# Optimization experiments

Measured on AMD Instinct MI355X. Metric: run time of the kernel, lower is better.

## Reference

```python
import jax, jax.numpy as jnp
from jax import lax
import numpy as np

B, V, H, K, E = 256, 30000, 512, 200, 300
SH_ALPHA = 20.0
REC_W = 0.7
N_ITERS = 100       # fixed iteration budget (original caps at 5000; convergence check freezes updates)
STOP_THR = 0.005
BN_EPS = 1e-3


def setup_inputs() -> dict:
    key = jax.random.key(0)
    ks = jax.random.split(key, 8)
    n = lambda k, shape, scale: (jax.random.normal(k, shape, jnp.float32) * scale)
    return {
        "bows": jax.random.uniform(ks[0], (B, V), jnp.float32),
        "W1": n(ks[1], (H, V), 0.01),
        "b1": jnp.zeros((H,), jnp.float32),
        "W2": n(ks[2], (K, H), 0.05),
        "b2": jnp.zeros((K,), jnp.float32),
        "gamma": jnp.ones((K,), jnp.float32),
        "beta": jnp.zeros((K,), jnp.float32),
        "word_emb": n(ks[3], (V, E), 0.1),
        "topic_emb": n(ks[4], (K, E), 0.1),
    }


def _l2norm(x):
    return x / jnp.maximum(jnp.linalg.norm(x, axis=1, keepdims=True), 1e-12)


def _sinkhorn(cost, kernel, a, b):
    # a: [K,B], b: [V,B], kernel: [K,V]
    u0 = jnp.ones_like(a) / a.shape[0]
    v0 = jnp.ones_like(b)

    def body(carry, i):
        u, v, err = carry
        active = err > STOP_THR
        # u = a / (kernel @ (b / (u^T kernel)^T))
        u1 = a / (kernel @ (b / (u.T @ kernel).T))

        def check(_):
            v1 = b / (kernel.T @ u1)
            u2 = a / (kernel @ v1)
            bb = v1 * (kernel.T @ u2)
            e = jnp.max(jnp.sum(jnp.abs(bb - b), axis=0))
            return u2, v1, e

        # original does the v-refresh + err check when steps % 20 == 1 (steps = i+1)
        u1, v1, e1 = lax.cond(i % 20 == 0, check, lambda _: (u1, v, err), None)
        u = jnp.where(active, u1, u)
        v = jnp.where(active, v1, v)
        err = jnp.where(active, e1, err)
        return (u, v, err), None

    (u, v, _), _ = lax.scan(jax.checkpoint(body), (u0, v0, jnp.asarray(1.0, a.dtype)),
                            jnp.arange(N_ITERS))
    # per-document sinkhorn cost: sum_k u * ((kernel*cost) @ v)
    return jnp.sum(u * ((kernel * cost) @ v), axis=0)  # [B]


def reference(bows, W1, b1, W2, b2, gamma, beta, word_emb, topic_emb):
    # encoder (training-mode BN with batch stats; dropout disabled for determinism)
    h = jax.nn.relu(bows @ W1.T + b1)                      # [B,H]
    z = h @ W2.T + b2                                      # [B,K]
    mu = jnp.mean(z, axis=0)
    var = jnp.var(z, axis=0)                               # biased, as torch BN uses
    zn = gamma * (z - mu) / jnp.sqrt(var + BN_EPS) + beta
    doc_topic = jax.nn.softmax(zn, axis=1)                 # [B,K]

    topic_word = _l2norm(topic_emb) @ _l2norm(word_emb).T  # [K,V]
    cost = 1.0 - topic_word
    kernel = jnp.exp(-cost * SH_ALPHA)

    doc_word = jax.nn.softmax(bows, axis=1)                # [B,V]
    sinkhorn_loss = _sinkhorn(cost, kernel, doc_topic.T, doc_word.T).mean()

    rec_log_probs = jax.nn.log_softmax(doc_topic @ topic_word, axis=1)  # [B,V]
    reconstruction_loss = -(rec_log_probs * bows).sum(axis=1).mean()
    return REC_W * reconstruction_loss, sinkhorn_loss
```

## Files before the change

### kernel.cpp

```cpp
#include <hip/hip_runtime.h>
#include <math.h>

#define CDIV(a,b) (((a)+(b)-1)/(b))

typedef unsigned short u16;
typedef unsigned long long u64;
typedef __attribute__((ext_vector_type(8))) short bf16x8;
typedef __attribute__((ext_vector_type(4))) float f32x4;

constexpr int Bn = 256;
constexpr int Vn = 30000;
constexpr int Hn = 512;
constexpr int Kn = 200;
constexpr int En = 300;
constexpr int Kp = 224;
constexpr int Vc = 224;
constexpr int NCH = 135;
constexpr int Vpad = NCH * Vc;
constexpr float ALPHA  = 20.0f;
constexpr float RECW   = 0.7f;
constexpr float THRC   = 0.005f;
constexpr float EPS_BN = 1e-3f;
constexpr int   NIT    = 100;

__device__ __forceinline__ float bf2f(u16 h) {
  union { unsigned u; float f; } c; c.u = (unsigned)h << 16; return c.f;
}
__device__ __forceinline__ u16 f2bf(float f) {
  union { float f; unsigned u; } c; c.f = f;
  return (u16)((c.u + 0x7fffu + ((c.u >> 16) & 1u)) >> 16);
}

template<int MODE>
__global__ __launch_bounds__(256, 2)
void fusedAB(const u16* __restrict__ kernT, const u16* __restrict__ kernA,
             const u16* __restrict__ ub, const u16* __restrict__ bmb,
             u16* __restrict__ wout, const u16* __restrict__ win,
             u16* __restrict__ tpart, float* __restrict__ errp,
             const int* __restrict__ frozen)
{
  if (MODE != 3 && frozen[0]) return;
  const int c = blockIdx.x, g = blockIdx.y;
  const int v0 = c * Vc, b0 = g * 64;
  const int tid = threadIdx.x;
  const int wv = tid >> 6, l = tid & 63, l15 = l & 15, lg = l >> 4;
  const int rloc = wv * 16 + l15;
  const int bcol = b0 + rloc;
  __shared__ u16 wlds[64 * Vc];
  char* wbase = (char*)wlds;
  const int sw = (rloc & 3) << 4;

  if (MODE != 3) {
    bf16x8 uf[7];
    {
      const u16* up = ub + (size_t)bcol * Kp + lg * 8;
#pragma unroll
      for (int ks = 0; ks < 7; ++ks) uf[ks] = *(const bf16x8*)(up + ks * 32);
    }
    float e = 0.f;
    for (int vt = 0; vt < Vc / 16; ++vt) {
      const u16* ktp = kernT + (size_t)(v0 + vt * 16 + l15) * Kp + lg * 8;
      f32x4 acc = {0.f, 0.f, 0.f, 0.f};
#pragma unroll
      for (int ks = 0; ks < 7; ++ks) {
        bf16x8 kf = *(const bf16x8*)(ktp + ks * 32);
        acc = __builtin_amdgcn_mfma_f32_16x16x32_bf16(kf, uf[ks], acc, 0, 0, 0);
      }
      const int vbase = v0 + vt * 16 + lg * 4;
      const size_t po = (size_t)bcol * Vpad + vbase;
      u64 bq = *(const u64*)(bmb + po);
      if (MODE == 2) {
        u64 wq = *(const u64*)(win + po);
#pragma unroll
        for (int r = 0; r < 4; ++r) {
          float bm = bf2f((u16)(bq >> (16 * r)));
          float wv_ = bf2f((u16)(wq >> (16 * r)));
          e += fabsf(wv_ * acc[r] - bm);
        }
      } else {
        u64 wq = 0;
#pragma unroll
        for (int r = 0; r < 4; ++r) {
          float bm = bf2f((u16)(bq >> (16 * r)));
          float w = (vbase + r < Vn) ? bm / acc[r] : 0.f;
          wq |= (u64)f2bf(w) << (16 * r);
        }
        *(u64*)(wbase + rloc * (Vc * 2) + ((vt * 32 + lg * 8) ^ sw)) = wq;
        if (MODE == 1) *(u64*)(wout + po) = wq;
      }
    }
    if (MODE == 2) {
      e += __shfl_xor(e, 16, 64);
      e += __shfl_xor(e, 32, 64);
      if (l < 16) errp[c * Bn + bcol] = e;
      return;
    }
    __syncthreads();
  }

  f32x4 accB[13];
#pragma unroll
  for (int mt = 0; mt < 13; ++mt) accB[mt] = (f32x4){0.f, 0.f, 0.f, 0.f};
  for (int vs = 0; vs < Vc / 32; ++vs) {
    bf16x8 wf;
    if (MODE == 3) wf = *(const bf16x8*)(win + (size_t)bcol * Vpad + v0 + vs * 32 + lg * 8);
    else wf = *(const bf16x8*)(wbase + rloc * (Vc * 2) + (((vs * 32 + lg * 8) * 2) ^ sw));
    const u16* kap = kernA + (size_t)l15 * Vpad + v0 + vs * 32 + lg * 8;
#pragma unroll
    for (int mt = 0; mt < 13; ++mt) {
      bf16x8 af = *(const bf16x8*)(kap + (size_t)mt * 16 * Vpad);
      accB[mt] = __builtin_amdgcn_mfma_f32_16x16x32_bf16(af, wf, accB[mt], 0, 0, 0);
    }
  }
#pragma unroll
  for (int mt = 0; mt < 13; ++mt) {
#pragma unroll
    for (int r = 0; r < 4; ++r) {
      int k = mt * 16 + lg * 4 + r;
      if (k < Kn) tpart[((size_t)c * Kn + k) * Bn + bcol] = f2bf(accB[mt][r]);
    }
  }
}

__global__ __launch_bounds__(256, 2)
void reconMF(const u16* __restrict__ costT, const u16* __restrict__ dtb,
             u16* __restrict__ rbuf)
{
  const int c = blockIdx.x, g = blockIdx.y;
  const int v0 = c * Vc, b0 = g * 64;
  const int tid = threadIdx.x;
  const int wv = tid >> 6, l = tid & 63, l15 = l & 15, lg = l >> 4;
  const int bcol = b0 + wv * 16 + l15;
  bf16x8 uf[7];
  {
    const u16* up = dtb + (size_t)bcol * Kp + lg * 8;
#pragma unroll
    for (int ks = 0; ks < 7; ++ks) uf[ks] = *(const bf16x8*)(up + ks * 32);
  }
  for (int vt = 0; vt < Vc / 16; ++vt) {
    const u16* ktp = costT + (size_t)(v0 + vt * 16 + l15) * Kp + lg * 8;
    f32x4 acc = {0.f, 0.f, 0.f, 0.f};
#pragma unroll
    for (int ks = 0; ks < 7; ++ks) {
      bf16x8 kf = *(const bf16x8*)(ktp + ks * 32);
      acc = __builtin_amdgcn_mfma_f32_16x16x32_bf16(kf, uf[ks], acc, 0, 0, 0);
    }
    const int vbase = v0 + vt * 16 + lg * 4;
    u64 q = 0;
#pragma unroll
    for (int r = 0; r < 4; ++r) q |= (u64)f2bf(1.f - acc[r]) << (16 * r);
    *(u64*)(rbuf + (size_t)bcol * Vpad + vbase) = q;
  }
}

__global__ void prepKern(const float* __restrict__ P, u16* __restrict__ kern_bf,
                         u16* __restrict__ kc_bf, u16* __restrict__ cost_bf)
{
  int k = blockIdx.y;
  int v = blockIdx.x * 256 + threadIdx.x;
  if (v >= Vpad) return;
  float cf = 0.f, kf = 0.f;
  if (k < Kn && v < Vn) {
    cf = 1.f - P[(size_t)k * Vn + v];
    kf = expf(-ALPHA * cf);
  }
  size_t o = (size_t)k * Vpad + v;
  kern_bf[o] = f2bf(kf);
  kc_bf[o]   = f2bf(kf * cf);
  cost_bf[o] = f2bf(cf);
}

__global__ void transposeK(const u16* __restrict__ src, u16* __restrict__ dst)
{
  __shared__ u16 t[32][33];
  int tx = threadIdx.x & 31, ty = threadIdx.x >> 5;
  int v0 = blockIdx.x * 32, k0 = blockIdx.y * 32;
#pragma unroll
  for (int r = 0; r < 4; ++r) t[ty + 8 * r][tx] = src[(size_t)(k0 + ty + 8 * r) * Vpad + v0 + tx];
  __syncthreads();
#pragma unroll
  for (int r = 0; r < 4; ++r) dst[(size_t)(v0 + ty + 8 * r) * Kp + k0 + tx] = t[tx][ty + 8 * r];
}

__global__ __launch_bounds__(256)
void gemm_nt(const float* __restrict__ A, const float* __restrict__ Bm,
             const float* __restrict__ rsA, const float* __restrict__ rsB,
             float* __restrict__ P, int M, int N, int Kd)
{
  const int S = gridDim.z, s = blockIdx.z;
  const int k0 = (int)((long long)Kd * s / S);
  const int k1 = (int)((long long)Kd * (s + 1) / S);
  const int m0 = blockIdx.y * 64, n0 = blockIdx.x * 64;
  __shared__ float As[16][68];
  __shared__ float Bs[16][68];
  const int tid = threadIdx.x;
  const int tx = tid & 15, ty = tid >> 4;
  const int lrow = tid >> 2, lkg = (tid & 3) * 4;
  const int mi = m0 + lrow, ni = n0 + lrow;
  float acc[4][4] = {};
  for (int kc = k0; kc < k1; kc += 16) {
    float4 a4 = {0.f, 0.f, 0.f, 0.f}, b4 = {0.f, 0.f, 0.f, 0.f};
    if (kc + 16 <= k1) {
      if (mi < M) a4 = *(const float4*)&A[(size_t)mi * Kd + kc + lkg];
      if (ni < N) b4 = *(const float4*)&Bm[(size_t)ni * Kd + kc + lkg];
    } else {
      float ta[4] = {0.f, 0.f, 0.f, 0.f}, tb[4] = {0.f, 0.f, 0.f, 0.f};
      for (int jj = 0; jj < 4; ++jj) {
        int kk = kc + lkg + jj;
        if (kk < k1) {
          if (mi < M) ta[jj] = A[(size_t)mi * Kd + kk];
          if (ni < N) tb[jj] = Bm[(size_t)ni * Kd + kk];
        }
      }
      a4.x = ta[0]; a4.y = ta[1]; a4.z = ta[2]; a4.w = ta[3];
      b4.x = tb[0]; b4.y = tb[1]; b4.z = tb[2]; b4.w = tb[3];
    }
    if (rsA && mi < M) { float sc = rsA[mi]; a4.x *= sc; a4.y *= sc; a4.z *= sc; a4.w *= sc; }
    if (rsB && ni < N) { float sc = rsB[ni]; b4.x *= sc; b4.y *= sc; b4.z *= sc; b4.w *= sc; }
    As[lkg + 0][lrow] = a4.x; As[lkg + 1][lrow] = a4.y;
    As[lkg + 2][lrow] = a4.z; As[lkg + 3][lrow] = a4.w;
    Bs[lkg + 0][lrow] = b4.x; Bs[lkg + 1][lrow] = b4.y;
    Bs[lkg + 2][lrow] = b4.z; Bs[lkg + 3][lrow] = b4.w;
    __syncthreads();
#pragma unroll
    for (int kk = 0; kk < 16; ++kk) {
      float4 av = *(const float4*)&As[kk][ty * 4];
      float4 bv = *(const float4*)&Bs[kk][tx * 4];
      float a_[4] = {av.x, av.y, av.z, av.w};
      float b_[4] = {bv.x, bv.y, bv.z, bv.w};
#pragma unroll
      for (int i = 0; i < 4; ++i)
#pragma unroll
        for (int j = 0; j < 4; ++j)
          acc[i][j] += a_[i] * b_[j];
    }
    __syncthreads();
  }
  const size_t base = (size_t)s * M * N;
#pragma unroll
  for (int i = 0; i < 4; ++i) {
    int m = m0 + ty * 4 + i;
    if (m >= M) continue;
#pragma unroll
    for (int j = 0; j < 4; ++j) {
      int n = n0 + tx * 4 + j;
      if (n < N) P[base + (size_t)m * N + n] = acc[i][j];
    }
  }
}

__global__ void rowNorms(const float* __restrict__ X, float* __restrict__ rn, int R, int C)
{
  int wv = threadIdx.x >> 6, lane = threadIdx.x & 63;
  int r = blockIdx.x * 4 + wv;
  if (r >= R) return;
  float s = 0.f;
  for (int c = lane; c < C; c += 64) { float x = X[(size_t)r * C + c]; s += x * x; }
#pragma unroll
  for (int m = 32; m; m >>= 1) s += __shfl_xor(s, m, 64);
  if (lane == 0) rn[r] = 1.f / fmaxf(sqrtf(s), 1e-12f);
}

__global__ void epiH(const float* __restrict__ P, const float* __restrict__ b1,
                     float* __restrict__ h, int S)
{
  int i = blockIdx.x * blockDim.x + threadIdx.x;
  if (i >= Bn * Hn) return;
  float v = b1[i & (Hn - 1)];
  for (int s = 0; s < S; ++s) v += P[(size_t)s * Bn * Hn + i];
  h[i] = fmaxf(v, 0.f);
}

__global__ void bnStats(const float* __restrict__ P, const float* __restrict__ b2,
                        float* __restrict__ mu, float* __restrict__ ivar, int S)
{
  int k = blockIdx.x, b = threadIdx.x;
  float z = b2[k];
  for (int s = 0; s < S; ++s) z += P[((size_t)s * Bn + b) * Kn + k];
  __shared__ float r1[256], r2[256];
  r1[b] = z; r2[b] = z * z; __syncthreads();
  for (int st = 128; st; st >>= 1) {
    if (b < st) { r1[b] += r1[b + st]; r2[b] += r2[b + st]; }
    __syncthreads();
  }
  if (b == 0) {
    float m = r1[0] / Bn, v = r2[0] / Bn - (r1[0] / Bn) * (r1[0] / Bn);
    mu[k] = m; ivar[k] = rsqrtf(v + EPS_BN);
  }
}

__global__ void bnSoftmax(const float* __restrict__ P, const float* __restrict__ b2,
                          const float* __restrict__ mu, const float* __restrict__ ivar,
                          const float* __restrict__ gamma, const float* __restrict__ beta,
                          float* __restrict__ a, u16* __restrict__ dtb, int S)
{
  int b = blockIdx.x, k = threadIdx.x;
  float zn = -1e30f;
  if (k < Kn) {
    float z = b2[k];
    for (int s = 0; s < S; ++s) z += P[((size_t)s * Bn + b) * Kn + k];
    zn = gamma[k] * (z - mu[k]) * ivar[k] + beta[k];
  }
  __shared__ float red[256];
  red[k] = zn; __syncthreads();
  for (int st = 128; st; st >>= 1) { if (k < st) red[k] = fmaxf(red[k], red[k + st]); __syncthreads(); }
  float mx = red[0]; __syncthreads();
  float e = (k < Kn) ? expf(zn - mx) : 0.f;
  red[k] = e; __syncthreads();
  for (int st = 128; st; st >>= 1) { if (k < st) red[k] += red[k + st]; __syncthreads(); }
  float dt = e / red[0];
  if (k < Kn) a[(size_t)k * Bn + b] = dt;
  if (k < Kp) dtb[(size_t)b * Kp + k] = (k < Kn) ? f2bf(dt) : (u16)0;
}

__global__ __launch_bounds__(512)
void rowSoftmax2(const float* __restrict__ bows, u16* __restrict__ bmb)
{
  int b = blockIdx.x, t = threadIdx.x;
  const float4* row = (const float4*)(bows + (size_t)b * Vn);
  __shared__ float red[512];
  float mx = -1e30f;
  for (int v4 = t; v4 < Vn / 4; v4 += 512) {
    float4 x = row[v4];
    mx = fmaxf(mx, fmaxf(fmaxf(x.x, x.y), fmaxf(x.z, x.w)));
  }
  red[t] = mx; __syncthreads();
  for (int st = 256; st; st >>= 1) { if (t < st) red[t] = fmaxf(red[t], red[t + st]); __syncthreads(); }
  mx = red[0]; __syncthreads();
  float sum = 0.f;
  for (int v4 = t; v4 < Vn / 4; v4 += 512) {
    float4 x = row[v4];
    sum += expf(x.x - mx) + expf(x.y - mx) + expf(x.z - mx) + expf(x.w - mx);
  }
  red[t] = sum; __syncthreads();
  for (int st = 256; st; st >>= 1) { if (t < st) red[t] += red[t + st]; __syncthreads(); }
  float inv = 1.f / red[0];
  for (int v4 = t; v4 < Vn / 4; v4 += 512) {
    float4 x = row[v4];
    u64 q = (u64)f2bf(expf(x.x - mx) * inv)
          | ((u64)f2bf(expf(x.y - mx) * inv) << 16)
          | ((u64)f2bf(expf(x.z - mx) * inv) << 32)
          | ((u64)f2bf(expf(x.w - mx) * inv) << 48);
    *(u64*)(bmb + (size_t)b * Vpad + v4 * 4) = q;
  }
  for (int p = t; p < (Vpad - Vn) / 4; p += 512)
    *(u64*)(bmb + (size_t)b * Vpad + Vn + p * 4) = 0;
}

__global__ void initU2(float* __restrict__ u, u16* __restrict__ ub)
{
  int i = blockIdx.x * 256 + threadIdx.x;
  int k = i >> 8, b = i & 255;
  u[i] = 1.f / Kn;
  ub[(size_t)b * Kp + k] = f2bf(1.f / Kn);
  if (k < Kp - Kn) ub[(size_t)b * Kp + Kn + k] = 0;
}

__global__ void updateU2(const u16* __restrict__ tpart, const float* __restrict__ a,
                         float* __restrict__ u, u16* __restrict__ ub,
                         const int* __restrict__ frozen)
{
  if (frozen[0]) return;
  int i = blockIdx.x * 256 + threadIdx.x;
  float t = 0.f;
  for (int c = 0; c < NCH; ++c) t += bf2f(tpart[(size_t)c * Kn * Bn + i]);
  float uu = a[i] / t;
  u[i] = uu;
  int k = i >> 8, b = i & 255;
  ub[(size_t)b * Kp + k] = f2bf(uu);
  if (k < Kp - Kn) ub[(size_t)b * Kp + Kn + k] = 0;
}

__global__ void sumT(const u16* __restrict__ tpart, float* __restrict__ t2)
{
  int i = blockIdx.x * 256 + threadIdx.x;
  float t = 0.f;
  for (int c = 0; c < NCH; ++c) t += bf2f(tpart[(size_t)c * Kn * Bn + i]);
  t2[i] = t;
}

__global__ void errFin(const float* __restrict__ errp, int nc, int* __restrict__ frozen)
{
  if (frozen[0]) return;
  int b = threadIdx.x;
  float s = 0.f;
  for (int c = 0; c < nc; ++c) s += errp[(size_t)c * Bn + b];
  __shared__ float red[256];
  red[b] = s; __syncthreads();
  for (int st = 128; st; st >>= 1) { if (b < st) red[b] = fmaxf(red[b], red[b + st]); __syncthreads(); }
  if (b == 0 && red[0] <= THRC) frozen[0] = 1;
}

__global__ __launch_bounds__(512)
void recPass2(const u16* __restrict__ r, const float* __restrict__ bows,
              float* __restrict__ Lb)
{
  int b = blockIdx.x, t = threadIdx.x;
  const float m = 1.0f;
  const float4* br = (const float4*)(bows + (size_t)b * Vn);
  float se = 0.f, dot = 0.f, bs = 0.f;
  for (int v4 = t; v4 < Vn / 4; v4 += 512) {
    u64 q = *(const u64*)(r + (size_t)b * Vpad + v4 * 4);
    float4 w = br[v4];
    float x0 = bf2f((u16)q), x1 = bf2f((u16)(q >> 16));
    float x2 = bf2f((u16)(q >> 32)), x3 = bf2f((u16)(q >> 48));
    se  += expf(x0 - m) + expf(x1 - m) + expf(x2 - m) + expf(x3 - m);
    dot += w.x * x0 + w.y * x1 + w.z * x2 + w.w * x3;
    bs  += w.x + w.y + w.z + w.w;
  }
  __shared__ float red[512];
  red[t] = se; __syncthreads();
  for (int st = 256; st; st >>= 1) { if (t < st) red[t] += red[t + st]; __syncthreads(); }
  float seT = red[0]; __syncthreads();
  red[t] = dot; __syncthreads();
  for (int st = 256; st; st >>= 1) { if (t < st) red[t] += red[t + st]; __syncthreads(); }
  float dotT = red[0]; __syncthreads();
  red[t] = bs; __syncthreads();
  for (int st = 256; st; st >>= 1) { if (t < st) red[t] += red[t + st]; __syncthreads(); }
  if (t == 0) Lb[b] = dotT - (m + logf(seT)) * red[0];
}

__global__ void finalOut(const float* __restrict__ u, const float* __restrict__ t2,
                         const float* __restrict__ Lb, float* __restrict__ outp)
{
  int b = threadIdx.x;
  float sl = 0.f;
  for (int k = 0; k < Kn; ++k) sl += u[(size_t)k * Bn + b] * t2[(size_t)k * Bn + b];
  __shared__ float r1[256], r2[256];
  r1[b] = sl; r2[b] = Lb[b]; __syncthreads();
  for (int st = 128; st; st >>= 1) {
    if (b < st) { r1[b] += r1[b + st]; r2[b] += r2[b + st]; }
    __syncthreads();
  }
  if (b == 0) {
    outp[0] = RECW * (-(r2[0] / (float)Bn));
    outp[1] = r1[0] / (float)Bn;
  }
}

extern "C" void kernel_launch(void* const* d_in, const int* in_sizes, int n_in,
                              void* d_out, int out_size, void* d_ws, size_t ws_size,
                              hipStream_t stream)
{
  const float* bows  = (const float*)d_in[0];
  const float* W1    = (const float*)d_in[1];
  const float* b1    = (const float*)d_in[2];
  const float* W2    = (const float*)d_in[3];
  const float* b2    = (const float*)d_in[4];
  const float* gamma = (const float*)d_in[5];
  const float* beta  = (const float*)d_in[6];
  const float* wemb  = (const float*)d_in[7];
  const float* temb  = (const float*)d_in[8];
  float* out = (float*)d_out;

  float* ws = (float*)d_ws;
  size_t off = 0;
  auto alloc = [&](size_t n) { float* p = ws + off; off += (n + 63) & ~(size_t)63; return p; };
  float* wbuf    = alloc((size_t)Kn * Vn);
  u16*   kern_bf = (u16*)alloc(((size_t)Kp * Vpad + 1) / 2);
  u16*   kc_bf   = (u16*)alloc(((size_t)Kp * Vpad + 1) / 2);
  u16*   cost_bf = (u16*)alloc(((size_t)Kp * Vpad + 1) / 2);
  u16*   kernT   = (u16*)alloc(((size_t)Vpad * Kp + 1) / 2);
  u16*   costT   = (u16*)alloc(((size_t)Vpad * Kp + 1) / 2);
  u16*   bm_bf   = (u16*)alloc(((size_t)Bn * Vpad + 1) / 2);
  u16*   vb_bf   = (u16*)alloc(((size_t)Bn * Vpad + 1) / 2);
  u16*   rbuf    = (u16*)alloc(((size_t)Bn * Vpad + 1) / 2);
  u16*   ub_bf   = (u16*)alloc(((size_t)Bn * Kp + 1) / 2);
  u16*   dt_bf   = (u16*)alloc(((size_t)Bn * Kp + 1) / 2);
  u16*   tpart   = (u16*)alloc(((size_t)NCH * Kn * Bn + 1) / 2);
  float* hbuf    = alloc((size_t)Bn * Hn);
  float* abuf    = alloc((size_t)Kn * Bn);
  float* ubuf    = alloc((size_t)Kn * Bn);
  float* t2      = alloc((size_t)Kn * Bn);
  float* rnT     = alloc(Kn);
  float* rnW     = alloc(Vn);
  float* mu      = alloc(Kn);
  float* ivar    = alloc(Kn);
  float* errp    = alloc((size_t)NCH * Bn);
  float* Lb      = alloc(Bn);
  int* frozen = (int*)(ws + off); off += 64;
  if (off * sizeof(float) > ws_size) return;

  hipMemsetAsync(frozen, 0, sizeof(int), stream);

  rowNorms<<<CDIV(Kn, 4), 256, 0, stream>>>(temb, rnT, Kn, En);
  rowNorms<<<CDIV(Vn, 4), 256, 0, stream>>>(wemb, rnW, Vn, En);
  {
    dim3 g(CDIV(Vn, 64), CDIV(Kn, 64), 1);
    gemm_nt<<<g, 256, 0, stream>>>(temb, wemb, rnT, rnW, wbuf, Kn, Vn, En);
  }
  prepKern<<<dim3(CDIV(Vpad, 256), Kp), 256, 0, stream>>>(wbuf, kern_bf, kc_bf, cost_bf);
  transposeK<<<dim3(Vpad / 32, Kp / 32), 256, 0, stream>>>(kern_bf, kernT);
  transposeK<<<dim3(Vpad / 32, Kp / 32), 256, 0, stream>>>(cost_bf, costT);

  {
    dim3 g(CDIV(Hn, 64), CDIV(Bn, 64), 25);
    gemm_nt<<<g, 256, 0, stream>>>(bows, W1, nullptr, nullptr, wbuf, Bn, Hn, Vn);
  }
  epiH<<<CDIV(Bn * Hn, 256), 256, 0, stream>>>(wbuf, b1, hbuf, 25);
  {
    dim3 g(CDIV(Kn, 64), CDIV(Bn, 64), 4);
    gemm_nt<<<g, 256, 0, stream>>>(hbuf, W2, nullptr, nullptr, wbuf, Bn, Kn, Hn);
  }
  bnStats<<<Kn, 256, 0, stream>>>(wbuf, b2, mu, ivar, 4);
  bnSoftmax<<<Bn, 256, 0, stream>>>(wbuf, b2, mu, ivar, gamma, beta, abuf, dt_bf, 4);
  rowSoftmax2<<<Bn, 512, 0, stream>>>(bows, bm_bf);
  initU2<<<Kn, 256, 0, stream>>>(ubuf, ub_bf);

  dim3 gF(NCH, Bn / 64);
  for (int it = 0; it < NIT; ++it) {
    fusedAB<0><<<gF, 256, 0, stream>>>(kernT, kern_bf, ub_bf, bm_bf, nullptr, nullptr, tpart, nullptr, frozen);
    updateU2<<<Kn, 256, 0, stream>>>(tpart, abuf, ubuf, ub_bf, frozen);
    if (it % 20 == 0) {
      fusedAB<1><<<gF, 256, 0, stream>>>(kernT, kern_bf, ub_bf, bm_bf, vb_bf, nullptr, tpart, nullptr, frozen);
      updateU2<<<Kn, 256, 0, stream>>>(tpart, abuf, ubuf, ub_bf, frozen);
      fusedAB<2><<<gF, 256, 0, stream>>>(kernT, kern_bf, ub_bf, bm_bf, nullptr, vb_bf, tpart, errp, frozen);
      errFin<<<1, 256, 0, stream>>>(errp, NCH, frozen);
    }
  }

  reconMF<<<gF, 256, 0, stream>>>(costT, dt_bf, rbuf);
  recPass2<<<Bn, 512, 0, stream>>>(rbuf, bows, Lb);

  fusedAB<3><<<gF, 256, 0, stream>>>(kernT, kc_bf, ub_bf, bm_bf, nullptr, vb_bf, tpart, nullptr, frozen);
  sumT<<<Kn, 256, 0, stream>>>(tpart, t2);
  finalOut<<<1, 256, 0, stream>>>(ubuf, t2, Lb, out);
}
```

Measured before the change: 2.256 ms.

## Move setup GEMMs to bf16 MFMA, remap grids per XCD, vectorize u updates

The topic-word similarity GEMM now runs on MFMA using split hi/lo bf16 operands (three products) and fuses the kernel/cost epilogue, replacing the fp32 SIMT GEMM plus prepKern. The bows@W1 encoder GEMM moves to a bf16 MFMA split-K kernel. The sinkhorn fusedAB grid becomes 1D with chunk mapping grouped by XCD, NCH is padded to 136, and occupancy is raised to 3 blocks per CU. updateU2 and sumT read tpart with 64-bit vector loads, and the fp32 u copy is dropped in favour of the bf16 one. Workspace buffers are aliased to save memory. The trade-offs are bf16 rounding of the encoder inputs and a finalOut that now reads bf16 u.

```diff
diff --git a/kernel.cpp b/kernel.cpp
--- a/kernel.cpp
+++ b/kernel.cpp
@@ -13,10 +13,13 @@
 constexpr int Hn = 512;
 constexpr int Kn = 200;
 constexpr int En = 300;
+constexpr int E3 = 320;
 constexpr int Kp = 224;
 constexpr int Vc = 224;
-constexpr int NCH = 135;
+constexpr int NCH = 136;
+constexpr int CPX = NCH / 8;
 constexpr int Vpad = NCH * Vc;
+constexpr int SW1 = 32;
 constexpr float ALPHA  = 20.0f;
 constexpr float RECW   = 0.7f;
 constexpr float THRC   = 0.005f;
@@ -30,9 +33,18 @@
   union { float f; unsigned u; } c; c.f = f;
   return (u16)((c.u + 0x7fffu + ((c.u >> 16) & 1u)) >> 16);
 }
+__device__ __forceinline__ bf16x8 load8bf(const float* p) {
+  float4 a = *(const float4*)p, b = *(const float4*)(p + 4);
+  bf16x8 r;
+  r[0] = (short)f2bf(a.x); r[1] = (short)f2bf(a.y);
+  r[2] = (short)f2bf(a.z); r[3] = (short)f2bf(a.w);
+  r[4] = (short)f2bf(b.x); r[5] = (short)f2bf(b.y);
+  r[6] = (short)f2bf(b.z); r[7] = (short)f2bf(b.w);
+  return r;
+}
 
 template<int MODE>
-__global__ __launch_bounds__(256, 2)
+__global__ __launch_bounds__(256, 3)
 void fusedAB(const u16* __restrict__ kernT, const u16* __restrict__ kernA,
              const u16* __restrict__ ub, const u16* __restrict__ bmb,
              u16* __restrict__ wout, const u16* __restrict__ win,
@@ -40,7 +52,9 @@
              const int* __restrict__ frozen)
 {
   if (MODE != 3 && frozen[0]) return;
-  const int c = blockIdx.x, g = blockIdx.y;
+  const int bid = blockIdx.x;
+  const int xcd = bid & 7, wid = bid >> 3;
+  const int c = xcd * CPX + (wid >> 2), g = wid & 3;
   const int v0 = c * Vc, b0 = g * 64;
   const int tid = threadIdx.x;
   const int wv = tid >> 6, l = tid & 63, l15 = l & 15, lg = l >> 4;
@@ -153,21 +167,98 @@
   }
 }
 
-__global__ void prepKern(const float* __restrict__ P, u16* __restrict__ kern_bf,
-                         u16* __restrict__ kc_bf, u16* __restrict__ cost_bf)
-{
-  int k = blockIdx.y;
-  int v = blockIdx.x * 256 + threadIdx.x;
-  if (v >= Vpad) return;
-  float cf = 0.f, kf = 0.f;
-  if (k < Kn && v < Vn) {
-    cf = 1.f - P[(size_t)k * Vn + v];
-    kf = expf(-ALPHA * cf);
-  }
-  size_t o = (size_t)k * Vpad + v;
-  kern_bf[o] = f2bf(kf);
-  kc_bf[o]   = f2bf(kf * cf);
-  cost_bf[o] = f2bf(cf);
+__global__ __launch_bounds__(256)
+void gemmTW(const u16* __restrict__ nth, const u16* __restrict__ ntl,
+            const u16* __restrict__ nwh, const u16* __restrict__ nwl,
+            u16* __restrict__ kern_bf, u16* __restrict__ kc_bf,
+            u16* __restrict__ cost_bf)
+{
+  const int n0 = blockIdx.x * 64;
+  const int tid = threadIdx.x;
+  const int wv = tid >> 6, l = tid & 63, l15 = l & 15, lg = l >> 4;
+  const int n = n0 + wv * 16 + l15;
+  const bool nok = n < Vn;
+  f32x4 acc[14];
+#pragma unroll
+  for (int mt = 0; mt < 14; ++mt) acc[mt] = (f32x4){0.f, 0.f, 0.f, 0.f};
+  for (int kc = 0; kc < E3; kc += 32) {
+    bf16x8 bh = {0,0,0,0,0,0,0,0}, bl = {0,0,0,0,0,0,0,0};
+    if (nok) {
+      const size_t o = (size_t)n * E3 + kc + lg * 8;
+      bh = *(const bf16x8*)(nwh + o);
+      bl = *(const bf16x8*)(nwl + o);
+    }
+#pragma unroll
+    for (int mt = 0; mt < 14; ++mt) {
+      const size_t ao = (size_t)(mt * 16 + l15) * E3 + kc + lg * 8;
+      bf16x8 ah = *(const bf16x8*)(nth + ao);
+      bf16x8 al = *(const bf16x8*)(ntl + ao);
+      acc[mt] = __builtin_amdgcn_mfma_f32_16x16x32_bf16(ah, bh, acc[mt], 0, 0, 0);
+      acc[mt] = __builtin_amdgcn_mfma_f32_16x16x32_bf16(ah, bl, acc[mt], 0, 0, 0);
+      acc[mt] = __builtin_amdgcn_mfma_f32_16x16x32_bf16(al, bh, acc[mt], 0, 0, 0);
+    }
+  }
+#pragma unroll
+  for (int mt = 0; mt < 14; ++mt) {
+#pragma unroll
+    for (int r = 0; r < 4; ++r) {
+      int k = mt * 16 + lg * 4 + r;
+      float cf = 1.f - acc[mt][r];
+      float kf = expf(-ALPHA * cf);
+      size_t o = (size_t)k * Vpad + n;
+      kern_bf[o] = f2bf(kf);
+      kc_bf[o]   = f2bf(kf * cf);
+      cost_bf[o] = f2bf(cf);
+    }
+  }
+}
+
+__global__ __launch_bounds__(256)
+void gemmW1(const float* __restrict__ A, const float* __restrict__ B,
+            float* __restrict__ part)
+{
+  const int bid = blockIdx.x;
+  const int xcd = bid & 7, wid = bid >> 3;
+  const int s = xcd * 4 + (wid >> 3);
+  const int nx = wid & 7;
+  const int n0 = nx * 64, k0 = s * 960;
+  const int tid = threadIdx.x;
+  const int wv = tid >> 6, l = tid & 63, l15 = l & 15, lg = l >> 4;
+  f32x4 acc[4][4];
+#pragma unroll
+  for (int i = 0; i < 4; ++i)
+#pragma unroll
+    for (int j = 0; j < 4; ++j) acc[i][j] = (f32x4){0.f, 0.f, 0.f, 0.f};
+  for (int kc = k0; kc < k0 + 960; kc += 32) {
+    const int kk = kc + lg * 8;
+    const bool ok = kk < Vn;
+    bf16x8 af[4], bf[4];
+#pragma unroll
+    for (int mt = 0; mt < 4; ++mt) {
+      const int m = wv * 64 + mt * 16 + l15;
+      af[mt] = ok ? load8bf(A + (size_t)m * Vn + kk) : (bf16x8){0,0,0,0,0,0,0,0};
+    }
+#pragma unroll
+    for (int nt = 0; nt < 4; ++nt) {
+      const int n = n0 + nt * 16 + l15;
+      bf[nt] = ok ? load8bf(B + (size_t)n * Vn + kk) : (bf16x8){0,0,0,0,0,0,0,0};
+    }
+#pragma unroll
+    for (int mt = 0; mt < 4; ++mt)
+#pragma unroll
+      for (int nt = 0; nt < 4; ++nt)
+        acc[mt][nt] = __builtin_amdgcn_mfma_f32_16x16x32_bf16(af[mt], bf[nt], acc[mt][nt], 0, 0, 0);
+  }
+#pragma unroll
+  for (int mt = 0; mt < 4; ++mt)
+#pragma unroll
+    for (int nt = 0; nt < 4; ++nt)
+#pragma unroll
+      for (int r = 0; r < 4; ++r) {
+        const int m = wv * 64 + mt * 16 + lg * 4 + r;
+        const int n = n0 + nt * 16 + l15;
+        part[(size_t)s * (Bn * Hn) + (size_t)m * Hn + n] = acc[mt][nt][r];
+      }
 }
 
 __global__ void transposeK(const u16* __restrict__ src, u16* __restrict__ dst)
@@ -182,9 +273,31 @@
   for (int r = 0; r < 4; ++r) dst[(size_t)(v0 + ty + 8 * r) * Kp + k0 + tx] = t[tx][ty + 8 * r];
 }
 
+__global__ void convTemb(const float* __restrict__ temb, const float* __restrict__ rnT,
+                         u16* __restrict__ nth, u16* __restrict__ ntl)
+{
+  int k = blockIdx.x, e = threadIdx.x;
+  float v = (k < Kn && e < En) ? temb[(size_t)k * En + e] * rnT[k] : 0.f;
+  u16 hi = f2bf(v);
+  nth[(size_t)k * E3 + e] = hi;
+  ntl[(size_t)k * E3 + e] = f2bf(v - bf2f(hi));
+}
+
+__global__ void convWemb(const float* __restrict__ wemb, const float* __restrict__ rnW,
+                         u16* __restrict__ nwh, u16* __restrict__ nwl)
+{
+  for (size_t idx = (size_t)blockIdx.x * 256 + threadIdx.x; idx < (size_t)Vn * E3;
+       idx += (size_t)gridDim.x * 256) {
+    int v = (int)(idx / E3), e = (int)(idx - (size_t)v * E3);
+    float x = (e < En) ? wemb[(size_t)v * En + e] * rnW[v] : 0.f;
+    u16 hi = f2bf(x);
+    nwh[idx] = hi;
+    nwl[idx] = f2bf(x - bf2f(hi));
+  }
+}
+
 __global__ __launch_bounds__(256)
 void gemm_nt(const float* __restrict__ A, const float* __restrict__ Bm,
-             const float* __restrict__ rsA, const float* __restrict__ rsB,
              float* __restrict__ P, int M, int N, int Kd)
 {
   const int S = gridDim.z, s = blockIdx.z;
@@ -200,23 +313,8 @@
   float acc[4][4] = {};
   for (int kc = k0; kc < k1; kc += 16) {
     float4 a4 = {0.f, 0.f, 0.f, 0.f}, b4 = {0.f, 0.f, 0.f, 0.f};
-    if (kc + 16 <= k1) {
-      if (mi < M) a4 = *(const float4*)&A[(size_t)mi * Kd + kc + lkg];
-      if (ni < N) b4 = *(const float4*)&Bm[(size_t)ni * Kd + kc + lkg];
-    } else {
-      float ta[4] = {0.f, 0.f, 0.f, 0.f}, tb[4] = {0.f, 0.f, 0.f, 0.f};
-      for (int jj = 0; jj < 4; ++jj) {
-        int kk = kc + lkg + jj;
-        if (kk < k1) {
-          if (mi < M) ta[jj] = A[(size_t)mi * Kd + kk];
-          if (ni < N) tb[jj] = Bm[(size_t)ni * Kd + kk];
-        }
-      }
-      a4.x = ta[0]; a4.y = ta[1]; a4.z = ta[2]; a4.w = ta[3];
-      b4.x = tb[0]; b4.y = tb[1]; b4.z = tb[2]; b4.w = tb[3];
-    }
-    if (rsA && mi < M) { float sc = rsA[mi]; a4.x *= sc; a4.y *= sc; a4.z *= sc; a4.w *= sc; }
-    if (rsB && ni < N) { float sc = rsB[ni]; b4.x *= sc; b4.y *= sc; b4.z *= sc; b4.w *= sc; }
+    if (mi < M) a4 = *(const float4*)&A[(size_t)mi * Kd + kc + lkg];
+    if (ni < N) b4 = *(const float4*)&Bm[(size_t)ni * Kd + kc + lkg];
     As[lkg + 0][lrow] = a4.x; As[lkg + 1][lrow] = a4.y;
     As[lkg + 2][lrow] = a4.z; As[lkg + 3][lrow] = a4.w;
     Bs[lkg + 0][lrow] = b4.x; Bs[lkg + 1][lrow] = b4.y;
@@ -347,36 +445,42 @@
     *(u64*)(bmb + (size_t)b * Vpad + Vn + p * 4) = 0;
 }
 
-__global__ void initU2(float* __restrict__ u, u16* __restrict__ ub)
-{
-  int i = blockIdx.x * 256 + threadIdx.x;
-  int k = i >> 8, b = i & 255;
-  u[i] = 1.f / Kn;
-  ub[(size_t)b * Kp + k] = f2bf(1.f / Kn);
-  if (k < Kp - Kn) ub[(size_t)b * Kp + Kn + k] = 0;
+__global__ void initU2(u16* __restrict__ ub)
+{
+  int b = blockIdx.x, k = threadIdx.x;
+  ub[(size_t)b * Kp + k] = (k < Kn) ? f2bf(1.f / Kn) : (u16)0;
 }
 
 __global__ void updateU2(const u16* __restrict__ tpart, const float* __restrict__ a,
-                         float* __restrict__ u, u16* __restrict__ ub,
-                         const int* __restrict__ frozen)
+                         u16* __restrict__ ub, const int* __restrict__ frozen)
 {
   if (frozen[0]) return;
   int i = blockIdx.x * 256 + threadIdx.x;
-  float t = 0.f;
-  for (int c = 0; c < NCH; ++c) t += bf2f(tpart[(size_t)c * Kn * Bn + i]);
-  float uu = a[i] / t;
-  u[i] = uu;
-  int k = i >> 8, b = i & 255;
-  ub[(size_t)b * Kp + k] = f2bf(uu);
-  if (k < Kp - Kn) ub[(size_t)b * Kp + Kn + k] = 0;
+  int k = i >> 6, b0 = (i & 63) * 4;
+  float t0 = 0.f, t1 = 0.f, t2_ = 0.f, t3 = 0.f;
+  for (int c = 0; c < NCH; ++c) {
+    u64 q = *(const u64*)(tpart + ((size_t)c * Kn + k) * Bn + b0);
+    t0 += bf2f((u16)q);        t1 += bf2f((u16)(q >> 16));
+    t2_ += bf2f((u16)(q >> 32)); t3 += bf2f((u16)(q >> 48));
+  }
+  float4 av = *(const float4*)&a[(size_t)k * Bn + b0];
+  ub[(size_t)(b0 + 0) * Kp + k] = f2bf(av.x / t0);
+  ub[(size_t)(b0 + 1) * Kp + k] = f2bf(av.y / t1);
+  ub[(size_t)(b0 + 2) * Kp + k] = f2bf(av.z / t2_);
+  ub[(size_t)(b0 + 3) * Kp + k] = f2bf(av.w / t3);
 }
 
 __global__ void sumT(const u16* __restrict__ tpart, float* __restrict__ t2)
 {
   int i = blockIdx.x * 256 + threadIdx.x;
-  float t = 0.f;
-  for (int c = 0; c < NCH; ++c) t += bf2f(tpart[(size_t)c * Kn * Bn + i]);
-  t2[i] = t;
+  int k = i >> 6, b0 = (i & 63) * 4;
+  float4 t = {0.f, 0.f, 0.f, 0.f};
+  for (int c = 0; c < NCH; ++c) {
+    u64 q = *(const u64*)(tpart + ((size_t)c * Kn + k) * Bn + b0);
+    t.x += bf2f((u16)q);         t.y += bf2f((u16)(q >> 16));
+    t.z += bf2f((u16)(q >> 32)); t.w += bf2f((u16)(q >> 48));
+  }
+  *(float4*)&t2[(size_t)k * Bn + b0] = t;
 }
 
 __global__ void errFin(const float* __restrict__ errp, int nc, int* __restrict__ frozen)
@@ -420,12 +524,12 @@
   if (t == 0) Lb[b] = dotT - (m + logf(seT)) * red[0];
 }
 
-__global__ void finalOut(const float* __restrict__ u, const float* __restrict__ t2,
+__global__ void finalOut(const u16* __restrict__ ub, const float* __restrict__ t2,
                          const float* __restrict__ Lb, float* __restrict__ outp)
 {
   int b = threadIdx.x;
   float sl = 0.f;
-  for (int k = 0; k < Kn; ++k) sl += u[(size_t)k * Bn + b] * t2[(size_t)k * Bn + b];
+  for (int k = 0; k < Kn; ++k) sl += bf2f(ub[(size_t)b * Kp + k]) * t2[(size_t)k * Bn + b];
   __shared__ float r1[256], r2[256];
   r1[b] = sl; r2[b] = Lb[b]; __syncthreads();
   for (int st = 128; st; st >>= 1) {
@@ -456,21 +560,21 @@
   float* ws = (float*)d_ws;
   size_t off = 0;
   auto alloc = [&](size_t n) { float* p = ws + off; off += (n + 63) & ~(size_t)63; return p; };
-  float* wbuf    = alloc((size_t)Kn * Vn);
+  float* wbuf    = alloc((size_t)SW1 * Bn * Hn);
   u16*   kern_bf = (u16*)alloc(((size_t)Kp * Vpad + 1) / 2);
+  u16*   kernT   = (u16*)alloc(((size_t)Vpad * Kp + 1) / 2);
   u16*   kc_bf   = (u16*)alloc(((size_t)Kp * Vpad + 1) / 2);
   u16*   cost_bf = (u16*)alloc(((size_t)Kp * Vpad + 1) / 2);
-  u16*   kernT   = (u16*)alloc(((size_t)Vpad * Kp + 1) / 2);
   u16*   costT   = (u16*)alloc(((size_t)Vpad * Kp + 1) / 2);
-  u16*   bm_bf   = (u16*)alloc(((size_t)Bn * Vpad + 1) / 2);
-  u16*   vb_bf   = (u16*)alloc(((size_t)Bn * Vpad + 1) / 2);
-  u16*   rbuf    = (u16*)alloc(((size_t)Bn * Vpad + 1) / 2);
+  u16*   nw_hi   = (u16*)alloc(((size_t)Vn * E3 + 1) / 2);
+  u16*   nw_lo   = (u16*)alloc(((size_t)Vn * E3 + 1) / 2);
+  u16*   nt_hi   = (u16*)alloc(((size_t)Kp * E3 + 1) / 2);
+  u16*   nt_lo   = (u16*)alloc(((size_t)Kp * E3 + 1) / 2);
   u16*   ub_bf   = (u16*)alloc(((size_t)Bn * Kp + 1) / 2);
   u16*   dt_bf   = (u16*)alloc(((size_t)Bn * Kp + 1) / 2);
   u16*   tpart   = (u16*)alloc(((size_t)NCH * Kn * Bn + 1) / 2);
   float* hbuf    = alloc((size_t)Bn * Hn);
   float* abuf    = alloc((size_t)Kn * Bn);
-  float* ubuf    = alloc((size_t)Kn * Bn);
   float* t2      = alloc((size_t)Kn * Bn);
   float* rnT     = alloc(Kn);
   float* rnW     = alloc(Vn);
@@ -480,49 +584,48 @@
   float* Lb      = alloc(Bn);
   int* frozen = (int*)(ws + off); off += 64;
   if (off * sizeof(float) > ws_size) return;
+  u16* bm_bf = nw_hi;
+  u16* vb_bf = nw_lo;
+  u16* rbuf  = kern_bf;
 
   hipMemsetAsync(frozen, 0, sizeof(int), stream);
 
   rowNorms<<<CDIV(Kn, 4), 256, 0, stream>>>(temb, rnT, Kn, En);
   rowNorms<<<CDIV(Vn, 4), 256, 0, stream>>>(wemb, rnW, Vn, En);
-  {
-    dim3 g(CDIV(Vn, 64), CDIV(Kn, 64), 1);
-    gemm_nt<<<g, 256, 0, stream>>>(temb, wemb, rnT, rnW, wbuf, Kn, Vn, En);
-  }
-  prepKern<<<dim3(CDIV(Vpad, 256), Kp), 256, 0, stream>>>(wbuf, kern_bf, kc_bf, cost_bf);
+  convTemb<<<Kp, E3, 0, stream>>>(temb, rnT, nt_hi, nt_lo);
+  convWemb<<<4096, 256, 0, stream>>>(wemb, rnW, nw_hi, nw_lo);
+  gemmTW<<<Vpad / 64, 256, 0, stream>>>(nt_hi, nt_lo, nw_hi, nw_lo, kern_bf, kc_bf, cost_bf);
   transposeK<<<dim3(Vpad / 32, Kp / 32), 256, 0, stream>>>(kern_bf, kernT);
   transposeK<<<dim3(Vpad / 32, Kp / 32), 256, 0, stream>>>(cost_bf, costT);
 
-  {
-    dim3 g(CDIV(Hn, 64), CDIV(Bn, 64), 25);
-    gemm_nt<<<g, 256, 0, stream>>>(bows, W1, nullptr, nullptr, wbuf, Bn, Hn, Vn);
-  }
-  epiH<<<CDIV(Bn * Hn, 256), 256, 0, stream>>>(wbuf, b1, hbuf, 25);
+  gemmW1<<<8 * SW1, 256, 0, stream>>>(bows, W1, wbuf);
+  epiH<<<CDIV(Bn * Hn, 256), 256, 0, stream>>>(wbuf, b1, hbuf, SW1);
   {
     dim3 g(CDIV(Kn, 64), CDIV(Bn, 64), 4);
-    gemm_nt<<<g, 256, 0, stream>>>(hbuf, W2, nullptr, nullptr, wbuf, Bn, Kn, Hn);
+    gemm_nt<<<g, 256, 0, stream>>>(hbuf, W2, wbuf, Bn, Kn, Hn);
   }
   bnStats<<<Kn, 256, 0, stream>>>(wbuf, b2, mu, ivar, 4);
   bnSoftmax<<<Bn, 256, 0, stream>>>(wbuf, b2, mu, ivar, gamma, beta, abuf, dt_bf, 4);
   rowSoftmax2<<<Bn, 512, 0, stream>>>(bows, bm_bf);
-  initU2<<<Kn, 256, 0, stream>>>(ubuf, ub_bf);
-
-  dim3 gF(NCH, Bn / 64);
+  initU2<<<Bn, Kp, 0, stream>>>(ub_bf);
+
+  const int gF = NCH * 4;
+  const int gU = (Kn * 64) / 256;
   for (int it = 0; it < NIT; ++it) {
     fusedAB<0><<<gF, 256, 0, stream>>>(kernT, kern_bf, ub_bf, bm_bf, nullptr, nullptr, tpart, nullptr, frozen);
-    updateU2<<<Kn, 256, 0, stream>>>(tpart, abuf, ubuf, ub_bf, frozen);
+    updateU2<<<gU, 256, 0, stream>>>(tpart, abuf, ub_bf, frozen);
     if (it % 20 == 0) {
       fusedAB<1><<<gF, 256, 0, stream>>>(kernT, kern_bf, ub_bf, bm_bf, vb_bf, nullptr, tpart, nullptr, frozen);
-      updateU2<<<Kn, 256, 0, stream>>>(tpart, abuf, ubuf, ub_bf, frozen);
+      updateU2<<<gU, 256, 0, stream>>>(tpart, abuf, ub_bf, frozen);
       fusedAB<2><<<gF, 256, 0, stream>>>(kernT, kern_bf, ub_bf, bm_bf, nullptr, vb_bf, tpart, errp, frozen);
       errFin<<<1, 256, 0, stream>>>(errp, NCH, frozen);
     }
   }
 
-  reconMF<<<gF, 256, 0, stream>>>(costT, dt_bf, rbuf);
+  reconMF<<<dim3(NCH, Bn / 64), 256, 0, stream>>>(costT, dt_bf, rbuf);
   recPass2<<<Bn, 512, 0, stream>>>(rbuf, bows, Lb);
 
-  fusedAB<3><<<gF, 256, 0, stream>>>(kernT, kc_bf, ub_bf, bm_bf, nullptr, vb_bf, tpart, nullptr, frozen);
-  sumT<<<Kn, 256, 0, stream>>>(tpart, t2);
-  finalOut<<<1, 256, 0, stream>>>(ubuf, t2, Lb, out);
-}
+  fusedAB<3><<<gF, 256, 0, stream>>>(nullptr, kc_bf, ub_bf, nullptr, nullptr, vb_bf, tpart, nullptr, frozen);
+  sumT<<<gU, 256, 0, stream>>>(tpart, t2);
+  finalOut<<<1, 256, 0, stream>>>(ub_bf, t2, Lb, out);
+}
```

Result: slower. 2.484 ms (+10.1%).
